# Kernel tuning notes

Hardware: AMD Instinct MI355X
Metric: run time of the kernel (lower is better)

## Reference

```python
import jax, jax.numpy as jnp
import numpy as np

NODES = 23   # 22 players + ball per frame-graph
K = 8        # random neighbors per node
B, T = 64, 128
G = B * T            # total graphs (frames)
N = G * NODES        # total nodes
D_IN, H, RH = 16, 128, 128


def setup_inputs() -> dict:
    key = jax.random.key(0)
    ks = jax.random.split(key, 10)
    x = jax.random.normal(ks[0], (N, D_IN), jnp.float32)
    # per-graph random edges: dst = each node repeated K times, src = random node in same graph
    src_local = jax.random.randint(ks[1], (G, NODES * K), 0, NODES)
    dst_local = jnp.tile(jnp.repeat(jnp.arange(NODES), K)[None, :], (G, 1))
    off = (jnp.arange(G) * NODES)[:, None]
    edge_index = jnp.stack([(src_local + off).reshape(-1),
                            (dst_local + off).reshape(-1)]).astype(jnp.int32)
    runner_idx = jax.random.randint(ks[2], (G,), 0, NODES, dtype=jnp.int32)
    sc = lambda k, sh: (jax.random.normal(k, sh, jnp.float32) * 0.05)
    return {
        'x': x, 'edge_index': edge_index, 'runner_idx': runner_idx,
        'W1': sc(ks[3], (D_IN, H)), 'b1': jnp.zeros((H,), jnp.float32),
        'W2': sc(ks[4], (H, H)),    'b2': jnp.zeros((H,), jnp.float32),
        'W_ih': sc(ks[5], (3 * RH, H)), 'W_hh': sc(ks[6], (3 * RH, RH)),
        'b_ih': jnp.zeros((3 * RH,), jnp.float32), 'b_hh': jnp.zeros((3 * RH,), jnp.float32),
        'Wp': sc(ks[7], (RH, 2)), 'bp': jnp.zeros((2,), jnp.float32),
    }


def _gcn_conv(h, edge_index, W, b):
    # PyG GCNConv: add self-loops, symmetric normalization, scatter-sum
    h = h @ W
    loop = jnp.arange(N, dtype=edge_index.dtype)
    s = jnp.concatenate([edge_index[0], loop])
    d = jnp.concatenate([edge_index[1], loop])
    deg = jax.ops.segment_sum(jnp.ones_like(s, h.dtype), d, num_segments=N)
    dinv = jnp.where(deg > 0, jax.lax.rsqrt(deg), 0.0)
    norm = dinv[s] * dinv[d]                      # [E+N]
    out = jax.ops.segment_sum(h[s] * norm[:, None], d, num_segments=N)
    return out + b


def _gru(seq, W_ih, W_hh, b_ih, b_hh):
    # torch GRU: gates in r,z,n order
    xg = seq @ W_ih.T + b_ih                      # [B,T,3RH]
    def step(hprev, xt):
        gh = hprev @ W_hh.T + b_hh
        xr, xz, xn = jnp.split(xt, 3, axis=-1)
        hr, hz, hn = jnp.split(gh, 3, axis=-1)
        r = jax.nn.sigmoid(xr + hr)
        z = jax.nn.sigmoid(xz + hz)
        n = jnp.tanh(xn + r * hn)
        hnew = (1.0 - z) * n + z * hprev
        return hnew, hnew
    h0 = jnp.zeros((seq.shape[0], RH), seq.dtype)
    _, outs = jax.lax.scan(step, h0, jnp.swapaxes(xg, 0, 1))
    return jnp.swapaxes(outs, 0, 1)               # [B,T,RH]


def reference(x, edge_index, runner_idx, W1, b1, W2, b2,
              W_ih, W_hh, b_ih, b_hh, Wp, bp):
    h = jax.nn.relu(_gcn_conv(x, edge_index, W1, b1))
    h = jax.nn.relu(_gcn_conv(h, edge_index, W2, b2))
    # fused equivalent of the per-graph nonzero()/indexing loop:
    runner_global = jnp.arange(G, dtype=jnp.int32) * NODES + runner_idx
    seq = h[runner_global].reshape(B, T, H)       # all lengths == T, padding is a no-op
    out = _gru(seq, W_ih, W_hh, b_ih, b_hh)
    return out @ Wp + bp                          # [B,T,2]
```

## Files before the change

kernel.cpp:

```cpp
#include <hip/hip_runtime.h>
#include <hip/hip_bf16.h>
#include <math.h>

#define GG 8192
#define NODESN 23
#define KK 8
#define DIN 16
#define HH 128
#define RHH 128
#define EPG (NODESN*KK)
#define TTT 128
#define BBB 64

__global__ __launch_bounds__(256) void gcn_hsum(
    const float* __restrict__ x, const int* __restrict__ esrc,
    const int* __restrict__ runner,
    const float* __restrict__ W1, const float* __restrict__ b1,
    float* __restrict__ hsum_g)
{
    __shared__ float xs[NODESN * DIN];
    __shared__ int   srcs[EPG];
    __shared__ float t1[NODESN * HH];
    __shared__ float red[256];

    const int g   = blockIdx.x;
    const int tid = threadIdx.x;
    const int j   = tid & 127;
    const int nh  = tid >> 7;

    for (int i = tid; i < NODESN * DIN; i += 256) xs[i] = x[g * NODESN * DIN + i];
    for (int i = tid; i < EPG; i += 256)          srcs[i] = esrc[g * EPG + i] - g * NODESN;

    float w[DIN];
    #pragma unroll
    for (int k = 0; k < DIN; k++) w[k] = W1[k * HH + j];
    const float b1j = b1[j];
    __syncthreads();

    const int n0 = nh * 12;
    const int n1 = nh ? NODESN : 12;
    for (int n = n0; n < n1; n++) {
        float acc = 0.f;
        #pragma unroll
        for (int k = 0; k < DIN; k += 4) {
            float4 xv = *(const float4*)&xs[n * DIN + k];
            acc = fmaf(xv.x, w[k], fmaf(xv.y, w[k+1], fmaf(xv.z, w[k+2], fmaf(xv.w, w[k+3], acc))));
        }
        t1[n * HH + j] = acc;
    }
    __syncthreads();

    const int r = runner[g];
    float part = 0.f;
    for (int slot = nh; slot < 9; slot += 2) {
        int node = (slot < 8) ? srcs[r * KK + slot] : r;
        float acc = t1[node * HH + j];
        #pragma unroll
        for (int k = 0; k < KK; k++) acc += t1[srcs[node * KK + k] * HH + j];
        part += fmaxf(acc * (1.f / 9.f) + b1j, 0.f);
    }
    red[tid] = part;
    __syncthreads();
    if (tid < HH) hsum_g[(size_t)g * HH + tid] = red[tid] + red[tid + 128];
}

__global__ __launch_bounds__(256) void seq_kernel(
    const float* __restrict__ hsum_g, const float* __restrict__ W2,
    const float* __restrict__ b2, float* __restrict__ seq)
{
    __shared__ float hs[16 * HH];
    const int tid = threadIdx.x;
    const int j = tid & 127, mh = tid >> 7;
    const size_t base = (size_t)blockIdx.x * 16 * HH;

    for (int v = tid; v < 16 * HH / 4; v += 256)
        ((float4*)hs)[v] = ((const float4*)(hsum_g + base))[v];
    __syncthreads();

    float acc[8];
    #pragma unroll
    for (int m = 0; m < 8; m++) acc[m] = 0.f;
    const float* hrow = hs + mh * 8 * HH;
    for (int k = 0; k < HH; k += 4) {
        float w0  = W2[(k+0)*HH + j];
        float w1  = W2[(k+1)*HH + j];
        float w2v = W2[(k+2)*HH + j];
        float w3  = W2[(k+3)*HH + j];
        #pragma unroll
        for (int m = 0; m < 8; m++) {
            float4 hv = *(const float4*)&hrow[m * HH + k];
            acc[m] = fmaf(hv.x, w0, fmaf(hv.y, w1, fmaf(hv.z, w2v, fmaf(hv.w, w3, acc[m]))));
        }
    }
    const float bj = b2[j];
    #pragma unroll
    for (int m = 0; m < 8; m++)
        seq[base + (size_t)(mh * 8 + m) * HH + j] = fmaxf(acc[m] * (1.f/9.f) + bj, 0.f);
}

__global__ void transpose_wih(const float* __restrict__ W, float* __restrict__ WT)
{
    int idx = blockIdx.x * 256 + threadIdx.x;
    if (idx < 3 * RHH * RHH) {
        int jj = idx / RHH, kk = idx - jj * RHH;
        WT[kk * (3 * RHH) + jj] = W[idx];
    }
}

__global__ __launch_bounds__(384) void xg_kernel(
    const float* __restrict__ seq, const float* __restrict__ WT,
    const float* __restrict__ b_ih, float* __restrict__ xg)
{
    const int tid = threadIdx.x;
    const int m0 = blockIdx.x * 8;
    const float* srow = seq + (size_t)m0 * RHH;
    float acc[8];
    const float bv = b_ih[tid];
    #pragma unroll
    for (int mi = 0; mi < 8; mi++) acc[mi] = bv;
    for (int k = 0; k < RHH; k += 4) {
        float w0 = WT[(k+0)*384 + tid];
        float w1 = WT[(k+1)*384 + tid];
        float w2 = WT[(k+2)*384 + tid];
        float w3 = WT[(k+3)*384 + tid];
        #pragma unroll
        for (int mi = 0; mi < 8; mi++) {
            float4 sv = *(const float4*)(srow + mi * RHH + k);
            acc[mi] = fmaf(sv.x, w0, fmaf(sv.y, w1, fmaf(sv.z, w2, fmaf(sv.w, w3, acc[mi]))));
        }
    }
    #pragma unroll
    for (int mi = 0; mi < 8; mi++)
        xg[(size_t)(m0 + mi) * 384 + tid] = acc[mi];
}

#define SMEM_FLOATS 20736
#define XG0 0
#define HB0 768

__global__ __launch_bounds__(1024)
__attribute__((amdgpu_waves_per_eu(4, 4)))
void gru_kernel(
    const float* __restrict__ xg, const float* __restrict__ W_hh,
    const float* __restrict__ b_hh, float* __restrict__ h_out)
{
    __shared__ float smem[SMEM_FLOATS];

    const int b    = blockIdx.x;
    const int tid  = threadIdx.x;
    const int lane = tid & 63;
    const int q    = lane >> 3;
    const int i    = ((tid >> 6) << 3) | (lane & 7);

    if (tid == 0) smem[SMEM_FLOATS - 1] = 0.f;

    float wr[16], wz[16], wn[16];
    int loff[4];
    {
        const float* br = W_hh + (size_t)i * RHH;
        const float* bz = br + (size_t)RHH * RHH;
        const float* bn = bz + (size_t)RHH * RHH;
        #pragma unroll
        for (int m = 0; m < 4; m++) {
            int p = (m + q) & 3;
            int o = q * 16 + 4 * p;
            loff[m] = o;
            float4 v;
            v = *(const float4*)(br + o); wr[4*m]=v.x; wr[4*m+1]=v.y; wr[4*m+2]=v.z; wr[4*m+3]=v.w;
            v = *(const float4*)(bz + o); wz[4*m]=v.x; wz[4*m+1]=v.y; wz[4*m+2]=v.z; wz[4*m+3]=v.w;
            v = *(const float4*)(bn + o); wn[4*m]=v.x; wn[4*m+1]=v.y; wn[4*m+2]=v.z; wn[4*m+3]=v.w;
        }
    }

    const float bhr = b_hh[i];
    const float bhz = b_hh[RHH + i];
    const float bhn = b_hh[2 * RHH + i];

    if (tid < HH) smem[HB0 + tid] = 0.f;
    const float* xbase = xg + (size_t)b * TTT * 3 * RHH;
    float xnext = 0.f;
    if (tid < 3 * RHH) {
        smem[XG0 + tid] = xbase[tid];
        xnext = xbase[3 * RHH + tid];
    }
    float hprev = 0.f;
    float* hob = h_out + (size_t)b * TTT * HH;
    __syncthreads();

    for (int t = 0; t < TTT; t++) {
        const float* hrow = &smem[HB0 + ((t & 1) << 7)];
        float ar = 0.f, az = 0.f, an = 0.f;
        #pragma unroll
        for (int m = 0; m < 4; m++) {
            float4 hv = *(const float4*)(hrow + loff[m]);
            ar = fmaf(hv.x, wr[4*m], fmaf(hv.y, wr[4*m+1], fmaf(hv.z, wr[4*m+2], fmaf(hv.w, wr[4*m+3], ar))));
            az = fmaf(hv.x, wz[4*m], fmaf(hv.y, wz[4*m+1], fmaf(hv.z, wz[4*m+2], fmaf(hv.w, wz[4*m+3], az))));
            an = fmaf(hv.x, wn[4*m], fmaf(hv.y, wn[4*m+1], fmaf(hv.z, wn[4*m+2], fmaf(hv.w, wn[4*m+3], an))));
        }

        if (tid < 3 * RHH) {
            smem[XG0 + (((t + 1) & 1) * 3 * RHH) + tid] = xnext;
            xnext = (t + 2 < TTT) ? xbase[(size_t)(t + 2) * 3 * RHH + tid] : 0.f;
        }

        ar += __shfl_xor(ar, 8); ar += __shfl_xor(ar, 16); ar += __shfl_xor(ar, 32);
        az += __shfl_xor(az, 8); az += __shfl_xor(az, 16); az += __shfl_xor(az, 32);
        an += __shfl_xor(an, 8); an += __shfl_xor(an, 16); an += __shfl_xor(an, 32);

        {
            const float* xr_s = &smem[XG0 + ((t & 1) * 3 * RHH)];
            float xr = xr_s[i], xz = xr_s[RHH + i], xn = xr_s[2 * RHH + i];
            float sr = xr + ar + bhr;
            float sz = xz + az + bhz;
            float rg = 1.f / (1.f + __expf(-sr));
            float zg = 1.f / (1.f + __expf(-sz));
            float tv = fmaf(rg, an + bhn, xn);
            tv = fminf(fmaxf(tv, -15.f), 15.f);
            float e2 = __expf(-2.f * tv);
            float ng = (1.f - e2) / (1.f + e2);
            hprev = fmaf(zg, hprev, (1.f - zg) * ng);
            if (q == 0) {
                smem[HB0 + (((t + 1) & 1) << 7) + i] = hprev;
                hob[t * HH + i] = hprev;
            }
        }
        __syncthreads();
    }
}

__global__ __launch_bounds__(256) void proj_kernel(
    const float* __restrict__ h_out, const float* __restrict__ Wp,
    const float* __restrict__ bp, float* __restrict__ out)
{
    __shared__ float wps[2 * RHH];
    __shared__ float bps[2];
    const int tid = threadIdx.x;
    if (tid < 2 * RHH) wps[tid] = Wp[tid];
    if (tid < 2) bps[tid] = bp[tid];
    __syncthreads();

    const int s = tid & 7;
    const int rl = tid >> 3;
    const size_t row = (size_t)blockIdx.x * 32 + rl;
    const float* hr = h_out + row * HH + s * 16;
    float a0 = 0.f, a1 = 0.f;
    #pragma unroll
    for (int m = 0; m < 16; m += 4) {
        float4 hv = *(const float4*)(hr + m);
        int k = s * 16 + m;
        a0 = fmaf(hv.x, wps[(k+0)*2], fmaf(hv.y, wps[(k+1)*2], fmaf(hv.z, wps[(k+2)*2], fmaf(hv.w, wps[(k+3)*2], a0))));
        a1 = fmaf(hv.x, wps[(k+0)*2+1], fmaf(hv.y, wps[(k+1)*2+1], fmaf(hv.z, wps[(k+2)*2+1], fmaf(hv.w, wps[(k+3)*2+1], a1))));
    }
    a0 += __shfl_xor(a0, 1); a0 += __shfl_xor(a0, 2); a0 += __shfl_xor(a0, 4);
    a1 += __shfl_xor(a1, 1); a1 += __shfl_xor(a1, 2); a1 += __shfl_xor(a1, 4);
    if (s == 0) {
        out[row * 2 + 0] = a0 + bps[0];
        out[row * 2 + 1] = a1 + bps[1];
    }
}

extern "C" void kernel_launch(void* const* d_in, const int* in_sizes, int n_in,
                              void* d_out, int out_size, void* d_ws, size_t ws_size,
                              hipStream_t stream)
{
    const float* x      = (const float*)d_in[0];
    const int*   eidx   = (const int*)d_in[1];
    const int*   runner = (const int*)d_in[2];
    const float* W1     = (const float*)d_in[3];
    const float* b1     = (const float*)d_in[4];
    const float* W2     = (const float*)d_in[5];
    const float* b2     = (const float*)d_in[6];
    const float* W_ih   = (const float*)d_in[7];
    const float* W_hh   = (const float*)d_in[8];
    const float* b_ih   = (const float*)d_in[9];
    const float* b_hh   = (const float*)d_in[10];
    const float* Wp     = (const float*)d_in[11];
    const float* bp     = (const float*)d_in[12];
    float* out = (float*)d_out;

    float* seq    = (float*)d_ws;
    float* xg     = seq + (size_t)GG * HH;
    float* WT     = xg + (size_t)GG * 3 * RHH;
    float* hsum_g = xg;
    float* h_out  = seq;

    transpose_wih<<<192, 256, 0, stream>>>(W_ih, WT);
    gcn_hsum<<<GG, 256, 0, stream>>>(x, eidx, runner, W1, b1, hsum_g);
    seq_kernel<<<GG / 16, 256, 0, stream>>>(hsum_g, W2, b2, seq);
    xg_kernel<<<GG / 8, 384, 0, stream>>>(seq, WT, b_ih, xg);
    gru_kernel<<<BBB, 1024, 0, stream>>>(xg, W_hh, b_hh, h_out);
    proj_kernel<<<GG / 32, 256, 0, stream>>>(h_out, Wp, bp, out);
}
```

Baseline: 276.3 us.

## Fuse output projection into GRU kernel and bulk-prefetch xg chunks into LDS

Folds the final 128->2 projection into the GRU kernel, so hidden states never round-trip through global memory and one launch goes away. The per-step register prefetch of xg is replaced by bulk loads of 64-timestep chunks into shared memory, taken off the recurrent critical path. Shared memory use grows to about 132KB per block, and each chunk boundary now waits on a bulk load that only 64 blocks issue. Empty asm statements pin the weights in registers.

```diff
diff --git a/kernel.cpp b/kernel.cpp
--- a/kernel.cpp
+++ b/kernel.cpp
@@ -134,25 +134,27 @@
         xg[(size_t)(m0 + mi) * 384 + tid] = acc[mi];
 }
 
-#define SMEM_FLOATS 20736
-#define XG0 0
-#define HB0 768
+#define CHUNK 64
+#define XGBUF_FLOATS (CHUNK * 3 * RHH)
+#define HOUT_FLOATS  (CHUNK * HH)
 
 __global__ __launch_bounds__(1024)
 __attribute__((amdgpu_waves_per_eu(4, 4)))
 void gru_kernel(
     const float* __restrict__ xg, const float* __restrict__ W_hh,
-    const float* __restrict__ b_hh, float* __restrict__ h_out)
-{
-    __shared__ float smem[SMEM_FLOATS];
+    const float* __restrict__ b_hh, const float* __restrict__ Wp,
+    const float* __restrict__ bp, float* __restrict__ out)
+{
+    __shared__ float xgbuf[XGBUF_FLOATS];
+    __shared__ float houtb[HOUT_FLOATS];
+    __shared__ float hpp[2 * HH];
+    __shared__ float wps[2 * RHH + 2];
 
     const int b    = blockIdx.x;
     const int tid  = threadIdx.x;
     const int lane = tid & 63;
     const int q    = lane >> 3;
     const int i    = ((tid >> 6) << 3) | (lane & 7);
-
-    if (tid == 0) smem[SMEM_FLOATS - 1] = 0.f;
 
     float wr[16], wz[16], wn[16];
     int loff[4];
@@ -171,91 +173,108 @@
             v = *(const float4*)(bn + o); wn[4*m]=v.x; wn[4*m+1]=v.y; wn[4*m+2]=v.z; wn[4*m+3]=v.w;
         }
     }
+    #pragma unroll
+    for (int m = 0; m < 16; m++) {
+        asm("" : "+v"(wr[m]));
+        asm("" : "+v"(wz[m]));
+        asm("" : "+v"(wn[m]));
+    }
 
     const float bhr = b_hh[i];
     const float bhz = b_hh[RHH + i];
     const float bhn = b_hh[2 * RHH + i];
 
-    if (tid < HH) smem[HB0 + tid] = 0.f;
+    if (tid < 2 * RHH) wps[tid] = Wp[tid];
+    if (tid < 2)       wps[2 * RHH + tid] = bp[tid];
+    if (tid < HH)      hpp[tid] = 0.f;
+    float hprev = 0.f;
+
     const float* xbase = xg + (size_t)b * TTT * 3 * RHH;
-    float xnext = 0.f;
-    if (tid < 3 * RHH) {
-        smem[XG0 + tid] = xbase[tid];
-        xnext = xbase[3 * RHH + tid];
-    }
-    float hprev = 0.f;
-    float* hob = h_out + (size_t)b * TTT * HH;
-    __syncthreads();
-
-    for (int t = 0; t < TTT; t++) {
-        const float* hrow = &smem[HB0 + ((t & 1) << 7)];
-        float ar = 0.f, az = 0.f, an = 0.f;
-        #pragma unroll
-        for (int m = 0; m < 4; m++) {
-            float4 hv = *(const float4*)(hrow + loff[m]);
-            ar = fmaf(hv.x, wr[4*m], fmaf(hv.y, wr[4*m+1], fmaf(hv.z, wr[4*m+2], fmaf(hv.w, wr[4*m+3], ar))));
-            az = fmaf(hv.x, wz[4*m], fmaf(hv.y, wz[4*m+1], fmaf(hv.z, wz[4*m+2], fmaf(hv.w, wz[4*m+3], az))));
-            an = fmaf(hv.x, wn[4*m], fmaf(hv.y, wn[4*m+1], fmaf(hv.z, wn[4*m+2], fmaf(hv.w, wn[4*m+3], an))));
-        }
-
-        if (tid < 3 * RHH) {
-            smem[XG0 + (((t + 1) & 1) * 3 * RHH) + tid] = xnext;
-            xnext = (t + 2 < TTT) ? xbase[(size_t)(t + 2) * 3 * RHH + tid] : 0.f;
-        }
-
-        ar += __shfl_xor(ar, 8); ar += __shfl_xor(ar, 16); ar += __shfl_xor(ar, 32);
-        az += __shfl_xor(az, 8); az += __shfl_xor(az, 16); az += __shfl_xor(az, 32);
-        an += __shfl_xor(an, 8); an += __shfl_xor(an, 16); an += __shfl_xor(an, 32);
-
+    float* outb = out + (size_t)b * TTT * 2;
+
+    for (int c = 0; c < TTT / CHUNK; c++) {
         {
-            const float* xr_s = &smem[XG0 + ((t & 1) * 3 * RHH)];
-            float xr = xr_s[i], xz = xr_s[RHH + i], xn = xr_s[2 * RHH + i];
-            float sr = xr + ar + bhr;
-            float sz = xz + az + bhz;
-            float rg = 1.f / (1.f + __expf(-sr));
-            float zg = 1.f / (1.f + __expf(-sz));
-            float tv = fmaf(rg, an + bhn, xn);
-            tv = fminf(fmaxf(tv, -15.f), 15.f);
-            float e2 = __expf(-2.f * tv);
-            float ng = (1.f - e2) / (1.f + e2);
-            hprev = fmaf(zg, hprev, (1.f - zg) * ng);
-            if (q == 0) {
-                smem[HB0 + (((t + 1) & 1) << 7) + i] = hprev;
-                hob[t * HH + i] = hprev;
+            const float4* src = (const float4*)(xbase + (size_t)c * XGBUF_FLOATS);
+            #pragma unroll
+            for (int v = 0; v < XGBUF_FLOATS / 4 / 1024; v++)
+                ((float4*)xgbuf)[tid + v * 1024] = src[tid + v * 1024];
+        }
+        if (c > 0) {
+            const int s  = tid & 7;
+            const int cc = (tid >> 3) & 1;
+            const int tl = tid >> 4;
+            const float* hr = &houtb[tl * HH + s * 16];
+            float acc = 0.f;
+            #pragma unroll
+            for (int m = 0; m < 16; m += 4) {
+                float4 hv = *(const float4*)(hr + m);
+                int k = s * 16 + m;
+                acc = fmaf(hv.x, wps[(k+0)*2 + cc],
+                      fmaf(hv.y, wps[(k+1)*2 + cc],
+                      fmaf(hv.z, wps[(k+2)*2 + cc],
+                      fmaf(hv.w, wps[(k+3)*2 + cc], acc))));
             }
+            acc += __shfl_xor(acc, 1); acc += __shfl_xor(acc, 2); acc += __shfl_xor(acc, 4);
+            if (s == 0)
+                outb[((c - 1) * CHUNK + tl) * 2 + cc] = acc + wps[2 * RHH + cc];
         }
         __syncthreads();
-    }
-}
-
-__global__ __launch_bounds__(256) void proj_kernel(
-    const float* __restrict__ h_out, const float* __restrict__ Wp,
-    const float* __restrict__ bp, float* __restrict__ out)
-{
-    __shared__ float wps[2 * RHH];
-    __shared__ float bps[2];
-    const int tid = threadIdx.x;
-    if (tid < 2 * RHH) wps[tid] = Wp[tid];
-    if (tid < 2) bps[tid] = bp[tid];
-    __syncthreads();
-
-    const int s = tid & 7;
-    const int rl = tid >> 3;
-    const size_t row = (size_t)blockIdx.x * 32 + rl;
-    const float* hr = h_out + row * HH + s * 16;
-    float a0 = 0.f, a1 = 0.f;
-    #pragma unroll
-    for (int m = 0; m < 16; m += 4) {
-        float4 hv = *(const float4*)(hr + m);
-        int k = s * 16 + m;
-        a0 = fmaf(hv.x, wps[(k+0)*2], fmaf(hv.y, wps[(k+1)*2], fmaf(hv.z, wps[(k+2)*2], fmaf(hv.w, wps[(k+3)*2], a0))));
-        a1 = fmaf(hv.x, wps[(k+0)*2+1], fmaf(hv.y, wps[(k+1)*2+1], fmaf(hv.z, wps[(k+2)*2+1], fmaf(hv.w, wps[(k+3)*2+1], a1))));
-    }
-    a0 += __shfl_xor(a0, 1); a0 += __shfl_xor(a0, 2); a0 += __shfl_xor(a0, 4);
-    a1 += __shfl_xor(a1, 1); a1 += __shfl_xor(a1, 2); a1 += __shfl_xor(a1, 4);
-    if (s == 0) {
-        out[row * 2 + 0] = a0 + bps[0];
-        out[row * 2 + 1] = a1 + bps[1];
+
+        for (int tl = 0; tl < CHUNK; tl++) {
+            const float* hrow = &hpp[(tl & 1) * HH];
+            float ar = 0.f, az = 0.f, an = 0.f;
+            #pragma unroll
+            for (int m = 0; m < 4; m++) {
+                float4 hv = *(const float4*)(hrow + loff[m]);
+                ar = fmaf(hv.x, wr[4*m], fmaf(hv.y, wr[4*m+1], fmaf(hv.z, wr[4*m+2], fmaf(hv.w, wr[4*m+3], ar))));
+                az = fmaf(hv.x, wz[4*m], fmaf(hv.y, wz[4*m+1], fmaf(hv.z, wz[4*m+2], fmaf(hv.w, wz[4*m+3], az))));
+                an = fmaf(hv.x, wn[4*m], fmaf(hv.y, wn[4*m+1], fmaf(hv.z, wn[4*m+2], fmaf(hv.w, wn[4*m+3], an))));
+            }
+
+            ar += __shfl_xor(ar, 8); ar += __shfl_xor(ar, 16); ar += __shfl_xor(ar, 32);
+            az += __shfl_xor(az, 8); az += __shfl_xor(az, 16); az += __shfl_xor(az, 32);
+            an += __shfl_xor(an, 8); an += __shfl_xor(an, 16); an += __shfl_xor(an, 32);
+
+            {
+                float xr = xgbuf[tl * 384 + i];
+                float xz = xgbuf[tl * 384 + RHH + i];
+                float xn = xgbuf[tl * 384 + 2 * RHH + i];
+                float sr = xr + ar + bhr;
+                float sz = xz + az + bhz;
+                float rg = 1.f / (1.f + __expf(-sr));
+                float zg = 1.f / (1.f + __expf(-sz));
+                float tv = fmaf(rg, an + bhn, xn);
+                tv = fminf(fmaxf(tv, -15.f), 15.f);
+                float e2 = __expf(-2.f * tv);
+                float ng = (1.f - e2) / (1.f + e2);
+                hprev = fmaf(zg, hprev, (1.f - zg) * ng);
+                if (q == 0) {
+                    hpp[((tl + 1) & 1) * HH + i] = hprev;
+                    houtb[tl * HH + i] = hprev;
+                }
+            }
+            __syncthreads();
+        }
+    }
+
+    {
+        const int s  = tid & 7;
+        const int cc = (tid >> 3) & 1;
+        const int tl = tid >> 4;
+        const float* hr = &houtb[tl * HH + s * 16];
+        float acc = 0.f;
+        #pragma unroll
+        for (int m = 0; m < 16; m += 4) {
+            float4 hv = *(const float4*)(hr + m);
+            int k = s * 16 + m;
+            acc = fmaf(hv.x, wps[(k+0)*2 + cc],
+                  fmaf(hv.y, wps[(k+1)*2 + cc],
+                  fmaf(hv.z, wps[(k+2)*2 + cc],
+                  fmaf(hv.w, wps[(k+3)*2 + cc], acc))));
+        }
+        acc += __shfl_xor(acc, 1); acc += __shfl_xor(acc, 2); acc += __shfl_xor(acc, 4);
+        if (s == 0)
+            outb[((TTT / CHUNK - 1) * CHUNK + tl) * 2 + cc] = acc + wps[2 * RHH + cc];
     }
 }
 
@@ -282,12 +301,10 @@
     float* xg     = seq + (size_t)GG * HH;
     float* WT     = xg + (size_t)GG * 3 * RHH;
     float* hsum_g = xg;
-    float* h_out  = seq;
 
     transpose_wih<<<192, 256, 0, stream>>>(W_ih, WT);
     gcn_hsum<<<GG, 256, 0, stream>>>(x, eidx, runner, W1, b1, hsum_g);
     seq_kernel<<<GG / 16, 256, 0, stream>>>(hsum_g, W2, b2, seq);
     xg_kernel<<<GG / 8, 384, 0, stream>>>(seq, WT, b_ih, xg);
-    gru_kernel<<<BBB, 1024, 0, stream>>>(xg, W_hh, b_hh, h_out);
-    proj_kernel<<<GG / 32, 256, 0, stream>>>(h_out, Wp, bp, out);
-}
+    gru_kernel<<<BBB, 1024, 0, stream>>>(xg, W_hh, b_hh, Wp, bp, out);
+}
```

New measurement: 273.0 us. About the same (-1.2%).
